# Kernel tuning notes

Hardware: AMD Instinct MI355X
Metric: run time of the kernel (lower is better)

## Reference

```python
import jax, jax.numpy as jnp
import numpy as np
from math import sqrt

DK = 64  # head dim from __init__ default


def setup_inputs() -> dict:
    key = jax.random.key(0)
    k1, k2, k3 = jax.random.split(key, 3)
    N, DV = 8192, 64
    Q = jax.random.normal(k1, (N, DK), dtype=jnp.float32)
    K = jax.random.normal(k2, (N, DK), dtype=jnp.float32)
    V = jax.random.normal(k3, (N, DV), dtype=jnp.float32)
    return {"Q": Q, "K": K, "V": V}


def reference(Q, K, V):
    # scores: [Nq, Nk]
    scores = jnp.einsum('qd,kd->qk', Q, K) * (1.0 / sqrt(DK))
    # softmax over key axis (torch nn.Softmax(dim=1) on 2D scores)
    attn = jax.nn.softmax(scores, axis=1)
    return jnp.einsum('qk,kv->qv', attn, V)
```

## Files before the change

### kernel.cpp

```cpp
#include <hip/hip_runtime.h>
#include <math.h>


typedef __bf16 bf16;
typedef __attribute__((ext_vector_type(4)))  __bf16 bf16x4;
typedef __attribute__((ext_vector_type(8)))  __bf16 bf16x8;
typedef __attribute__((ext_vector_type(16))) float  f32x16;

#define DKc 64
#define DVc 64
#define TK  64
#define QW  32
#define NW  4
#define QB  (QW * NW)

__device__ __forceinline__ f32x16 mfma_bf16(bf16x8 a, bf16x8 b, f32x16 c) {
    return __builtin_amdgcn_mfma_f32_32x32x16_bf16(a, b, c, 0, 0, 0);
}

__global__ __launch_bounds__(256, 2)
void attn_fwd_mfma(const float* __restrict__ Q, const float* __restrict__ K,
                   const float* __restrict__ V,
                   float* __restrict__ Opart, float* __restrict__ Mpart,
                   float* __restrict__ Lpart, float* __restrict__ Out,
                   int N, int splits, int chunk) {
    __shared__ __align__(16) short sK[TK * DKc];
    __shared__ __align__(16) short sV[DVc * TK];

    const int tid  = threadIdx.x;
    const int wid  = tid >> 6;
    const int lane = tid & 63;
    const int l31  = lane & 31;
    const int h    = lane >> 5;

    const int qbase = blockIdx.x * QB + wid * QW;
    const int q     = qbase + l31;
    const int sp    = blockIdx.y;

    bf16x8 qf[4];
#pragma unroll
    for (int f = 0; f < 4; ++f) {
        const float* qp = Q + (size_t)q * DKc + f * 16 + h * 8;
        float4 a = *(const float4*)qp;
        float4 b = *(const float4*)(qp + 4);
        qf[f][0] = (bf16)(a.x * 0.125f); qf[f][1] = (bf16)(a.y * 0.125f);
        qf[f][2] = (bf16)(a.z * 0.125f); qf[f][3] = (bf16)(a.w * 0.125f);
        qf[f][4] = (bf16)(b.x * 0.125f); qf[f][5] = (bf16)(b.y * 0.125f);
        qf[f][6] = (bf16)(b.z * 0.125f); qf[f][7] = (bf16)(b.w * 0.125f);
    }

    f32x16 O0 = {0}, O1 = {0};
    float m = -1e30f, lsum = 0.f;

    const int k0 = sp * chunk;
    int k1 = k0 + chunk; if (k1 > N) k1 = N;

    for (int t0 = k0; t0 < k1; t0 += TK) {
        __syncthreads();
#pragma unroll
        for (int it = 0; it < 4; ++it) {
            int idx = it * 256 + tid;
            int key = idx >> 4;
            int dk4 = (idx & 15) * 4;
            float4 kv = *(const float4*)(K + (size_t)(t0 + key) * DKc + dk4);
            bf16x4 w; w[0]=(bf16)kv.x; w[1]=(bf16)kv.y; w[2]=(bf16)kv.z; w[3]=(bf16)kv.w;
            int byte = ((key * DKc + dk4) * 2) ^ ((key & 7) << 4);
            *(bf16x4*)((char*)sK + byte) = w;
        }
        {
            int dv = tid & 63, kg = tid >> 6;
            union { bf16 s[16]; bf16x8 v8[2]; } u;
#pragma unroll
            for (int r = 0; r < 16; ++r) {
                float vv = V[(size_t)(t0 + kg * 16 + r) * DVc + dv];
                int rp = ((r >> 2) & 1) * 8 + (r & 3) + ((r >> 3) << 2);
                u.s[rp] = (bf16)vv;
            }
            int b0 = (dv * TK + kg * 16) * 2;
            int sw = (dv & 7) << 4;
            *(bf16x8*)((char*)sV + (b0 ^ sw))        = u.v8[0];
            *(bf16x8*)((char*)sV + ((b0 + 16) ^ sw)) = u.v8[1];
        }
        __syncthreads();

        f32x16 d0 = {0}, d1 = {0};
#pragma unroll
        for (int f = 0; f < 4; ++f) {
            int keyA = l31, keyB = 32 + l31;
            int ba = ((keyA * DKc * 2) + f * 32 + h * 16) ^ ((keyA & 7) << 4);
            int bb = ((keyB * DKc * 2) + f * 32 + h * 16) ^ ((keyB & 7) << 4);
            bf16x8 kf0 = *(const bf16x8*)((char*)sK + ba);
            bf16x8 kf1 = *(const bf16x8*)((char*)sK + bb);
            d0 = mfma_bf16(kf0, qf[f], d0);
            d1 = mfma_bf16(kf1, qf[f], d1);
        }

        float tm = -1e30f;
#pragma unroll
        for (int r = 0; r < 16; ++r) tm = fmaxf(tm, fmaxf(d0[r], d1[r]));
        tm = fmaxf(tm, __shfl_xor(tm, 32));
        float mn = fmaxf(m, tm);
        float fscale = __expf(m - mn);
        m = mn;

        float psum = 0.f;
#pragma unroll
        for (int r = 0; r < 16; ++r) {
            d0[r] = __expf(d0[r] - mn); psum += d0[r];
            d1[r] = __expf(d1[r] - mn); psum += d1[r];
        }
        psum += __shfl_xor(psum, 32);
        lsum = lsum * fscale + psum;

        bf16x8 pa[4];
#pragma unroll
        for (int j = 0; j < 8; ++j) {
            pa[0][j] = (bf16)d0[j];
            pa[1][j] = (bf16)d0[8 + j];
            pa[2][j] = (bf16)d1[j];
            pa[3][j] = (bf16)d1[8 + j];
        }

#pragma unroll
        for (int r = 0; r < 16; ++r) {
            int qr = (r & 3) + 8 * (r >> 2) + 4 * h;
            float fr = __shfl(fscale, (lane & 32) | qr);
            O0[r] *= fr; O1[r] *= fr;
        }

#pragma unroll
        for (int kb = 0; kb < 4; ++kb) {
            int dvA = l31, dvB = 32 + l31;
            int ba = ((dvA * TK * 2) + kb * 32 + h * 16) ^ ((dvA & 7) << 4);
            int bb = ((dvB * TK * 2) + kb * 32 + h * 16) ^ ((dvB & 7) << 4);
            bf16x8 vf0 = *(const bf16x8*)((char*)sV + ba);
            bf16x8 vf1 = *(const bf16x8*)((char*)sV + bb);
            O0 = mfma_bf16(pa[kb], vf0, O0);
            O1 = mfma_bf16(pa[kb], vf1, O1);
        }
    }

    if (splits == 1) {
        float inv = 1.f / lsum;
#pragma unroll
        for (int r = 0; r < 16; ++r) {
            int qr = (r & 3) + 8 * (r >> 2) + 4 * h;
            float fr = __shfl(inv, (lane & 32) | qr);
            int qq = qbase + qr;
            Out[(size_t)qq * DVc + l31]      = O0[r] * fr;
            Out[(size_t)qq * DVc + 32 + l31] = O1[r] * fr;
        }
    } else {
#pragma unroll
        for (int r = 0; r < 16; ++r) {
            int qr = (r & 3) + 8 * (r >> 2) + 4 * h;
            int qq = qbase + qr;
            size_t off = ((size_t)sp * N + qq) * DVc;
            Opart[off + l31]      = O0[r];
            Opart[off + 32 + l31] = O1[r];
        }
        if (lane < 32) {
            Mpart[(size_t)sp * N + q] = m;
            Lpart[(size_t)sp * N + q] = lsum;
        }
    }
}

__global__ __launch_bounds__(256)
void attn_combine(const float* __restrict__ Opart, const float* __restrict__ Mpart,
                  const float* __restrict__ Lpart, float* __restrict__ Out,
                  int N, int splits) {
    const int t  = blockIdx.x * blockDim.x + threadIdx.x;
    const int q  = t >> 4;
    const int d4 = t & 15;

    float M = -1e30f;
    for (int s = 0; s < splits; ++s) M = fmaxf(M, Mpart[(size_t)s * N + q]);

    float4 acc = make_float4(0.f, 0.f, 0.f, 0.f);
    float  L = 0.f;
    for (int s = 0; s < splits; ++s) {
        float w = __expf(Mpart[(size_t)s * N + q] - M);
        L += w * Lpart[(size_t)s * N + q];
        float4 ov = *(const float4*)(Opart + ((size_t)s * N + q) * DVc + d4 * 4);
        acc.x += w * ov.x; acc.y += w * ov.y; acc.z += w * ov.z; acc.w += w * ov.w;
    }
    float inv = 1.f / L;
    *(float4*)(Out + (size_t)q * DVc + d4 * 4) =
        make_float4(acc.x * inv, acc.y * inv, acc.z * inv, acc.w * inv);
}

extern "C" void kernel_launch(void* const* d_in, const int* in_sizes, int n_in,
                              void* d_out, int out_size, void* d_ws, size_t ws_size,
                              hipStream_t stream) {
    const float* Q = (const float*)d_in[0];
    const float* K = (const float*)d_in[1];
    const float* V = (const float*)d_in[2];
    float* Out = (float*)d_out;

    const int N = in_sizes[0] / DKc;

    int splits = 8;
    while (splits > 1 &&
           (size_t)splits * (size_t)N * (DVc + 2) * sizeof(float) > ws_size)
        splits >>= 1;
    int chunk = (N + splits - 1) / splits;
    chunk = ((chunk + TK - 1) / TK) * TK;

    float* Opart = (float*)d_ws;
    float* Mpart = Opart + (size_t)splits * N * DVc;
    float* Lpart = Mpart + (size_t)splits * N;

    dim3 grid(N / QB, splits);
    attn_fwd_mfma<<<grid, 256, 0, stream>>>(Q, K, V, Opart, Mpart, Lpart, Out,
                                            N, splits, chunk);
    if (splits > 1) {
        int total = N * 16;
        attn_combine<<<total / 256, 256, 0, stream>>>(Opart, Mpart, Lpart, Out,
                                                      N, splits);
    }
}
```

Before: 110.1 us.

## Precast Q/K/V to bf16 in a prepass and stream tiles via global_load_lds

Adds a prepass kernel that converts Q (pre-scaled by scale·log2e), K and a transposed, permuted V to bf16 in workspace. The main kernel then fills LDS with direct global-to-LDS DMA loads, with no per-tile conversion work. It also switches to exp2, skips the O rescale unless the running max rises by more than a threshold, doubles splits to 16 and raises the occupancy hint. The costs are an extra launch, extra workspace traffic and a lazy-rescale trick that lets the exponentials exceed 1.

New measurement: 100.6 us. 1.1x faster.

```diff
diff --git a/kernel.cpp b/kernel.cpp
--- a/kernel.cpp
+++ b/kernel.cpp
@@ -13,14 +13,63 @@
 #define QW  32
 #define NW  4
 #define QB  (QW * NW)
+#define SCALE_LOG2E 0.1803368801111204f
 
 __device__ __forceinline__ f32x16 mfma_bf16(bf16x8 a, bf16x8 b, f32x16 c) {
     return __builtin_amdgcn_mfma_f32_32x32x16_bf16(a, b, c, 0, 0, 0);
 }
-
-__global__ __launch_bounds__(256, 2)
-void attn_fwd_mfma(const float* __restrict__ Q, const float* __restrict__ K,
-                   const float* __restrict__ V,
+__device__ __forceinline__ int rp4(int r) {
+    return ((r >> 2) & 1) * 8 + (r & 3) + ((r >> 3) << 2);
+}
+
+__global__ __launch_bounds__(256)
+void prepass(const float* __restrict__ Q, const float* __restrict__ K,
+             const float* __restrict__ V,
+             bf16* __restrict__ Qb, bf16* __restrict__ Kb, bf16* __restrict__ Vt,
+             int N) {
+    const int b = blockIdx.x, tid = threadIdx.x;
+    const int nqb = (N * DKc) / (256 * 4);
+    if (b < 2 * nqb) {
+        bool isQ = b < nqb;
+        int idx = (isQ ? b : b - nqb) * 256 + tid;
+        float4 v = (isQ ? (const float4*)Q : (const float4*)K)[idx];
+        float sc = isQ ? SCALE_LOG2E : 1.0f;
+        bf16x4 w;
+        w[0] = (bf16)(v.x * sc); w[1] = (bf16)(v.y * sc);
+        w[2] = (bf16)(v.z * sc); w[3] = (bf16)(v.w * sc);
+        ((bf16x4*)(isQ ? Qb : Kb))[idx] = w;
+    } else {
+        const int T = b - 2 * nqb;
+        __shared__ float sT[64][65];
+#pragma unroll
+        for (int p = 0; p < 4; ++p) {
+            int fi = p * 256 + tid;
+            int e0 = fi * 4;
+            int key = e0 >> 6, dv = e0 & 63;
+            float4 v = ((const float4*)(V + (size_t)T * 64 * DVc))[fi];
+            sT[dv + 0][key] = v.x; sT[dv + 1][key] = v.y;
+            sT[dv + 2][key] = v.z; sT[dv + 3][key] = v.w;
+        }
+        __syncthreads();
+#pragma unroll
+        for (int w = 0; w < 2; ++w) {
+            int vidx = w * 256 + tid;
+            int dv = vidx >> 3, j0 = (vidx & 7) * 8;
+            bf16x8 o;
+#pragma unroll
+            for (int i = 0; i < 8; ++i) {
+                int j = j0 + i;
+                int ks = (j & 48) | rp4(j & 15);
+                o[i] = (bf16)sT[dv][ks];
+            }
+            *(bf16x8*)(Vt + (size_t)dv * N + T * 64 + j0) = o;
+        }
+    }
+}
+
+__global__ __launch_bounds__(256, 4)
+void attn_fwd_mfma(const bf16* __restrict__ Qb, const bf16* __restrict__ Kb,
+                   const bf16* __restrict__ Vt,
                    float* __restrict__ Opart, float* __restrict__ Mpart,
                    float* __restrict__ Lpart, float* __restrict__ Out,
                    int N, int splits, int chunk) {
@@ -39,15 +88,8 @@
 
     bf16x8 qf[4];
 #pragma unroll
-    for (int f = 0; f < 4; ++f) {
-        const float* qp = Q + (size_t)q * DKc + f * 16 + h * 8;
-        float4 a = *(const float4*)qp;
-        float4 b = *(const float4*)(qp + 4);
-        qf[f][0] = (bf16)(a.x * 0.125f); qf[f][1] = (bf16)(a.y * 0.125f);
-        qf[f][2] = (bf16)(a.z * 0.125f); qf[f][3] = (bf16)(a.w * 0.125f);
-        qf[f][4] = (bf16)(b.x * 0.125f); qf[f][5] = (bf16)(b.y * 0.125f);
-        qf[f][6] = (bf16)(b.z * 0.125f); qf[f][7] = (bf16)(b.w * 0.125f);
-    }
+    for (int f = 0; f < 4; ++f)
+        qf[f] = *(const bf16x8*)(Qb + (size_t)q * DKc + f * 16 + h * 8);
 
     f32x16 O0 = {0}, O1 = {0};
     float m = -1e30f, lsum = 0.f;
@@ -55,31 +97,34 @@
     const int k0 = sp * chunk;
     int k1 = k0 + chunk; if (k1 > N) k1 = N;
 
+    const char* KbB = (const char*)Kb;
+    const char* VtB = (const char*)Vt;
+    char* sKc = (char*)sK;
+    char* sVc = (char*)sV;
+    const size_t vrow = (size_t)N * 2;
+
     for (int t0 = k0; t0 < k1; t0 += TK) {
         __syncthreads();
 #pragma unroll
-        for (int it = 0; it < 4; ++it) {
-            int idx = it * 256 + tid;
-            int key = idx >> 4;
-            int dk4 = (idx & 15) * 4;
-            float4 kv = *(const float4*)(K + (size_t)(t0 + key) * DKc + dk4);
-            bf16x4 w; w[0]=(bf16)kv.x; w[1]=(bf16)kv.y; w[2]=(bf16)kv.z; w[3]=(bf16)kv.w;
-            int byte = ((key * DKc + dk4) * 2) ^ ((key & 7) << 4);
-            *(bf16x4*)((char*)sK + byte) = w;
-        }
-        {
-            int dv = tid & 63, kg = tid >> 6;
-            union { bf16 s[16]; bf16x8 v8[2]; } u;
-#pragma unroll
-            for (int r = 0; r < 16; ++r) {
-                float vv = V[(size_t)(t0 + kg * 16 + r) * DVc + dv];
-                int rp = ((r >> 2) & 1) * 8 + (r & 3) + ((r >> 3) << 2);
-                u.s[rp] = (bf16)vv;
-            }
-            int b0 = (dv * TK + kg * 16) * 2;
-            int sw = (dv & 7) << 4;
-            *(bf16x8*)((char*)sV + (b0 ^ sw))        = u.v8[0];
-            *(bf16x8*)((char*)sV + ((b0 + 16) ^ sw)) = u.v8[1];
+        for (int p = 0; p < 2; ++p) {
+            int o   = p * 4096 + wid * 1024 + lane * 16;
+            int key = o >> 7;
+            int so  = o ^ ((key & 7) << 4);
+            __builtin_amdgcn_global_load_lds(
+                (const __attribute__((address_space(1))) void*)(KbB + (size_t)t0 * 128 + so),
+                (__attribute__((address_space(3))) void*)(sKc + p * 4096 + wid * 1024),
+                16, 0, 0);
+        }
+#pragma unroll
+        for (int p = 0; p < 2; ++p) {
+            int o  = p * 4096 + wid * 1024 + lane * 16;
+            int dv = o >> 7;
+            int kb = o & 127;
+            int so = kb ^ ((dv & 7) << 4);
+            __builtin_amdgcn_global_load_lds(
+                (const __attribute__((address_space(1))) void*)(VtB + (size_t)dv * vrow + (size_t)t0 * 2 + so),
+                (__attribute__((address_space(3))) void*)(sVc + p * 4096 + wid * 1024),
+                16, 0, 0);
         }
         __syncthreads();
 
@@ -87,10 +132,10 @@
 #pragma unroll
         for (int f = 0; f < 4; ++f) {
             int keyA = l31, keyB = 32 + l31;
-            int ba = ((keyA * DKc * 2) + f * 32 + h * 16) ^ ((keyA & 7) << 4);
-            int bb = ((keyB * DKc * 2) + f * 32 + h * 16) ^ ((keyB & 7) << 4);
-            bf16x8 kf0 = *(const bf16x8*)((char*)sK + ba);
-            bf16x8 kf1 = *(const bf16x8*)((char*)sK + bb);
+            int ba = ((keyA * 128) + f * 32 + h * 16) ^ ((keyA & 7) << 4);
+            int bb = ((keyB * 128) + f * 32 + h * 16) ^ ((keyB & 7) << 4);
+            bf16x8 kf0 = *(const bf16x8*)(sKc + ba);
+            bf16x8 kf1 = *(const bf16x8*)(sKc + bb);
             d0 = mfma_bf16(kf0, qf[f], d0);
             d1 = mfma_bf16(kf1, qf[f], d1);
         }
@@ -99,18 +144,28 @@
 #pragma unroll
         for (int r = 0; r < 16; ++r) tm = fmaxf(tm, fmaxf(d0[r], d1[r]));
         tm = fmaxf(tm, __shfl_xor(tm, 32));
-        float mn = fmaxf(m, tm);
-        float fscale = __expf(m - mn);
-        m = mn;
+
+        float fs = 1.f;
+        if (__any(tm > m + 10.f)) {
+            float mn = fmaxf(m, tm);
+            fs = __builtin_amdgcn_exp2f(m - mn);
+            m = mn;
+#pragma unroll
+            for (int r = 0; r < 16; ++r) {
+                int qr = (r & 3) + 8 * (r >> 2) + 4 * h;
+                float fr = __shfl(fs, (lane & 32) | qr);
+                O0[r] *= fr; O1[r] *= fr;
+            }
+        }
 
         float psum = 0.f;
 #pragma unroll
         for (int r = 0; r < 16; ++r) {
-            d0[r] = __expf(d0[r] - mn); psum += d0[r];
-            d1[r] = __expf(d1[r] - mn); psum += d1[r];
+            d0[r] = __builtin_amdgcn_exp2f(d0[r] - m); psum += d0[r];
+            d1[r] = __builtin_amdgcn_exp2f(d1[r] - m); psum += d1[r];
         }
         psum += __shfl_xor(psum, 32);
-        lsum = lsum * fscale + psum;
+        lsum = lsum * fs + psum;
 
         bf16x8 pa[4];
 #pragma unroll
@@ -122,19 +177,12 @@
         }
 
 #pragma unroll
-        for (int r = 0; r < 16; ++r) {
-            int qr = (r & 3) + 8 * (r >> 2) + 4 * h;
-            float fr = __shfl(fscale, (lane & 32) | qr);
-            O0[r] *= fr; O1[r] *= fr;
-        }
-
-#pragma unroll
         for (int kb = 0; kb < 4; ++kb) {
             int dvA = l31, dvB = 32 + l31;
-            int ba = ((dvA * TK * 2) + kb * 32 + h * 16) ^ ((dvA & 7) << 4);
-            int bb = ((dvB * TK * 2) + kb * 32 + h * 16) ^ ((dvB & 7) << 4);
-            bf16x8 vf0 = *(const bf16x8*)((char*)sV + ba);
-            bf16x8 vf1 = *(const bf16x8*)((char*)sV + bb);
+            int ba = ((dvA * 128) + kb * 32 + h * 16) ^ ((dvA & 7) << 4);
+            int bb = ((dvB * 128) + kb * 32 + h * 16) ^ ((dvB & 7) << 4);
+            bf16x8 vf0 = *(const bf16x8*)(sVc + ba);
+            bf16x8 vf1 = *(const bf16x8*)(sVc + bb);
             O0 = mfma_bf16(pa[kb], vf0, O0);
             O1 = mfma_bf16(pa[kb], vf1, O1);
         }
@@ -180,7 +228,7 @@
     float4 acc = make_float4(0.f, 0.f, 0.f, 0.f);
     float  L = 0.f;
     for (int s = 0; s < splits; ++s) {
-        float w = __expf(Mpart[(size_t)s * N + q] - M);
+        float w = __builtin_amdgcn_exp2f(Mpart[(size_t)s * N + q] - M);
         L += w * Lpart[(size_t)s * N + q];
         float4 ov = *(const float4*)(Opart + ((size_t)s * N + q) * DVc + d4 * 4);
         acc.x += w * ov.x; acc.y += w * ov.y; acc.z += w * ov.z; acc.w += w * ov.w;
@@ -200,19 +248,29 @@
 
     const int N = in_sizes[0] / DKc;
 
-    int splits = 8;
+    const size_t bfbytes = (size_t)N * DKc * sizeof(short);
+    bf16* Qb = (bf16*)d_ws;
+    bf16* Kb = (bf16*)((char*)d_ws + bfbytes);
+    bf16* Vt = (bf16*)((char*)d_ws + 2 * bfbytes);
+    char* rest = (char*)d_ws + 3 * bfbytes;
+    size_t rest_sz = (ws_size > 3 * bfbytes) ? ws_size - 3 * bfbytes : 0;
+
+    int splits = 16;
     while (splits > 1 &&
-           (size_t)splits * (size_t)N * (DVc + 2) * sizeof(float) > ws_size)
+           (size_t)splits * (size_t)N * (DVc + 2) * sizeof(float) > rest_sz)
         splits >>= 1;
     int chunk = (N + splits - 1) / splits;
     chunk = ((chunk + TK - 1) / TK) * TK;
 
-    float* Opart = (float*)d_ws;
+    float* Opart = (float*)rest;
     float* Mpart = Opart + (size_t)splits * N * DVc;
     float* Lpart = Mpart + (size_t)splits * N;
 
+    const int nqb = (N * DKc) / (256 * 4);
+    prepass<<<2 * nqb + N / TK, 256, 0, stream>>>(Q, K, V, Qb, Kb, Vt, N);
+
     dim3 grid(N / QB, splits);
-    attn_fwd_mfma<<<grid, 256, 0, stream>>>(Q, K, V, Opart, Mpart, Lpart, Out,
+    attn_fwd_mfma<<<grid, 256, 0, stream>>>(Qb, Kb, Vt, Opart, Mpart, Lpart, Out,
                                             N, splits, chunk);
     if (splits > 1) {
         int total = N * 16;
```
